# Performance work log

Measured on AMD Instinct MI355X. Metric: run time of the kernel, lower is better.

Reference implementation:

```python
import jax, jax.numpy as jnp
import numpy as np

# pool sizes (must match init_kwargs)
N_FQK, N_FV, N_REL, N_VAL, N_KNOW = 512, 256, 128, 32, 256
K_FQK, K_FV, K_REL, K_VAL = 64, 32, 16, 3
D_MODEL, D_SPACE = 1024, 64
B, S = 8, 2048


def _topk_sparsify(w, k):
    # keep top-k entries per row, zero the rest (values unchanged)
    vals, idx = jax.lax.top_k(w, k)                      # [B,k]
    out = jnp.zeros_like(w)
    rows = jnp.arange(w.shape[0])[:, None]
    return out.at[rows, idx].set(vals), idx


def setup_inputs() -> dict:
    key = jax.random.key(0)
    k1, k2, k3, k4 = jax.random.split(key, 4)
    x = jax.random.normal(k1, (B, S, D_MODEL), dtype=jnp.float32)
    # importance: per-token weights normalized over sequence
    importance = jax.nn.softmax(jax.random.normal(k2, (B, S), dtype=jnp.float32), axis=-1)
    W = jax.random.normal(k3, (D_MODEL, D_SPACE), dtype=jnp.float32) * 0.02
    b = jnp.zeros((D_SPACE,), dtype=jnp.float32)
    total = N_FQK + N_FV + N_REL + N_VAL + N_KNOW
    neuron_emb = jax.random.normal(k4, (total, D_SPACE), dtype=jnp.float32) * 0.02
    return {"x": x, "importance": importance, "W": W, "b": b, "neuron_emb": neuron_emb}


def reference(x, importance, W, b, neuron_emb):
    # projection (dropout inactive in eval); normalized neuron embeddings
    h = x @ W + b                                         # [B,S,d_space]
    emb_n = neuron_emb / jnp.linalg.norm(neuron_emb, axis=-1, keepdims=True)
    all_logits = jnp.einsum('bsd,nd->bsn', h, emb_n)      # [B,S,N_total]

    e0 = N_FQK
    e1 = e0 + N_FV
    e2 = e1 + N_REL
    e3 = e2 + N_VAL

    def route(lo, hi):
        pref = jax.nn.softmax(all_logits[..., lo:hi], axis=-1)  # [B,S,n]
        w = jnp.einsum('bs,bsn->bn', importance, pref)          # [B,n]
        return pref, w

    _, w_qk = route(0, e0)
    _, idx_qk = jax.lax.top_k(w_qk, K_FQK)
    idx_qk = jnp.sort(idx_qk, axis=-1)

    _, w_v = route(e0, e1)
    _, idx_v = jax.lax.top_k(w_v, K_FV)
    idx_v = jnp.sort(idx_v, axis=-1)

    # relational Q and K share the same logit slice (eval: no excitability bonus)
    _, w_rQ = route(e1, e2)
    _, w_rK = route(e1, e2)
    rw_Q, _ = _topk_sparsify(w_rQ, K_REL)
    rw_K, _ = _topk_sparsify(w_rK, K_REL)

    _, w_val = route(e2, e3)
    vw, _ = _topk_sparsify(w_val, K_VAL)

    return idx_qk, idx_v, rw_Q, rw_K, vw, w_qk, w_v
```

## Files before the change

kernel.cpp:

```cpp
#include <hip/hip_runtime.h>
#include <hip/hip_bf16.h>
#include <hip/hip_fp16.h>
#include <math.h>

#define ROWS  16384
#define DM    1024
#define DS    64
#define NUSE  928
#define NPAD  960
#define RPB   16
#define NBLK  (ROWS/RPB)

typedef __attribute__((ext_vector_type(8))) short bf16x8;
typedef __attribute__((ext_vector_type(4))) float f32x4;

static __device__ inline f32x4 mfma16(bf16x8 a, bf16x8 b, f32x4 c) {
    return __builtin_amdgcn_mfma_f32_16x16x32_bf16(a, b, c, 0, 0, 0);
}

static __device__ inline void bfsplit(float v, unsigned short& h, unsigned short& l) {
    unsigned u = __float_as_uint(v);
    unsigned hr = u + 0x7FFFu + ((u >> 16) & 1u);
    h = (unsigned short)(hr >> 16);
    float hf = __uint_as_float((unsigned)h << 16);
    float r = v - hf;
    unsigned ur = __float_as_uint(r);
    unsigned lr2 = ur + 0x7FFFu + ((ur >> 16) & 1u);
    l = (unsigned short)(lr2 >> 16);
}

#define OFF_EBH  0LL
#define OFF_EBL  122880LL
#define OFF_WBH  245760LL
#define OFF_WBL  376832LL
#define OFF_WP   507904LL

__global__ __launch_bounds__(256) void k_prep(const float* __restrict__ emb,
                                              const float* __restrict__ W,
                                              unsigned short* __restrict__ ebh,
                                              unsigned short* __restrict__ ebl,
                                              unsigned short* __restrict__ wbh,
                                              unsigned short* __restrict__ wbl) {
    if (blockIdx.x < 4) {
        int n = blockIdx.x * 256 + threadIdx.x;
        if (n >= NPAD) return;
        if (n >= NUSE) {
            #pragma unroll
            for (int d = 0; d < DS; d++) {
                int kt = d >> 5, q = (d >> 3) & 3, j = d & 7;
                int a = ((kt * 4 + q) * NPAD + n) * 8 + j;
                ebh[a] = 0; ebl[a] = 0;
            }
            return;
        }
        float ss = 0.f;
        #pragma unroll
        for (int d = 0; d < DS; d++) { float v = emb[n * DS + d]; ss = fmaf(v, v, ss); }
        float inv = 1.0f / sqrtf(ss);
        #pragma unroll
        for (int d = 0; d < DS; d++) {
            float v = emb[n * DS + d] * inv;
            unsigned short h, l; bfsplit(v, h, l);
            int kt = d >> 5, q = (d >> 3) & 3, j = d & 7;
            int a = ((kt * 4 + q) * NPAD + n) * 8 + j;
            ebh[a] = h; ebl[a] = l;
        }
    } else {
        int idx = (blockIdx.x - 4) * 256 + threadIdx.x;
        int ktg = idx >> 6, n = idx & 63;
        #pragma unroll
        for (int q = 0; q < 4; q++) {
            #pragma unroll
            for (int j = 0; j < 8; j++) {
                int k = ktg * 32 + q * 8 + j;
                float v = W[k * DS + n];
                unsigned short h, l; bfsplit(v, h, l);
                int a = ((ktg * 4 + q) * 64 + n) * 8 + j;
                wbh[a] = h; wbl[a] = l;
            }
        }
    }
}

__global__ __launch_bounds__(512, 8) void k_mega(const float* __restrict__ x,
                                                 const float* __restrict__ bias,
                                                 const unsigned short* __restrict__ wbh,
                                                 const unsigned short* __restrict__ wbl,
                                                 const unsigned short* __restrict__ ebh,
                                                 const unsigned short* __restrict__ ebl,
                                                 const float* __restrict__ imp,
                                                 float* __restrict__ wpart) {
    __shared__ __align__(16) unsigned char smem[40960];
    unsigned short* Ph   = (unsigned short*)smem;
    float*          Cb   = (float*)smem;
    unsigned short* Hh   = (unsigned short*)(smem + 34560);
    unsigned short* Hl   = (unsigned short*)(smem + 36608);
    float*          zslot = (float*)(smem + 38656);
    float*          coefL = (float*)(smem + 40704);

    const int tid = threadIdx.x;
    const int rc = blockIdx.x;
    const long long row0 = (long long)rc * RPB;
    const int w = tid >> 6, lane = tid & 63, q = lane >> 4, lm = lane & 15;

    zslot[tid] = 0.f;

    {
        const int kg = w;
        const float* xp = &x[(row0 + lm) * (long long)DM + kg * 128 + q * 8];
        f32x4 acc[4];
        #pragma unroll
        for (int f = 0; f < 4; f++) { acc[f].x = 0.f; acc[f].y = 0.f; acc[f].z = 0.f; acc[f].w = 0.f; }

        #pragma unroll
        for (int ks = 0; ks < 4; ks++) {
            float4 v0 = *(const float4*)&xp[ks * 32];
            float4 v1 = *(const float4*)&xp[ks * 32 + 4];
            union { bf16x8 v; unsigned short s[8]; } ah, al;
            bfsplit(v0.x, ah.s[0], al.s[0]); bfsplit(v0.y, ah.s[1], al.s[1]);
            bfsplit(v0.z, ah.s[2], al.s[2]); bfsplit(v0.w, ah.s[3], al.s[3]);
            bfsplit(v1.x, ah.s[4], al.s[4]); bfsplit(v1.y, ah.s[5], al.s[5]);
            bfsplit(v1.z, ah.s[6], al.s[6]); bfsplit(v1.w, ah.s[7], al.s[7]);
            const int ktg = kg * 4 + ks;
            #pragma unroll
            for (int f = 0; f < 4; f++) {
                const int ba = ((ktg * 4 + q) * 64 + f * 16 + lm) * 8;
                const bf16x8 b_h = *(const bf16x8*)&wbh[ba];
                const bf16x8 b_l = *(const bf16x8*)&wbl[ba];
                acc[f] = mfma16(ah.v, b_h, acc[f]);
                acc[f] = mfma16(ah.v, b_l, acc[f]);
                acc[f] = mfma16(al.v, b_h, acc[f]);
            }
        }
        #pragma unroll
        for (int f = 0; f < 4; f++)
            *(f32x4*)&Cb[(w * 64 + lane) * 16 + f * 4] = acc[f];
    }
    __syncthreads();

    #pragma unroll
    for (int ee = 0; ee < 2; ee++) {
        const int e = tid * 2 + ee;
        float s = 0.f;
        #pragma unroll
        for (int g = 0; g < 8; g++) s += Cb[g * 1024 + e];
        const int L = e >> 4, r = e & 15, f = r >> 2, t = r & 3;
        const int row = (L >> 4) * 4 + t;
        const int col = f * 16 + (L & 15);
        s += bias[col];
        unsigned short hh, ll; bfsplit(s, hh, ll);
        const int kt = col >> 5, qH = (col >> 3) & 3, j = col & 7;
        const int hidx = ((kt * 4 + qH) * RPB + row) * 8 + j;
        Hh[hidx] = hh; Hl[hidx] = ll;
    }
    __syncthreads();

    bf16x8 a_h[2], a_l[2];
    #pragma unroll
    for (int kt = 0; kt < 2; kt++) {
        const int ab = ((kt * 4 + q) * RPB + lm) * 8;
        a_h[kt] = *(const bf16x8*)&Hh[ab];
        a_l[kt] = *(const bf16x8*)&Hl[ab];
    }

    #pragma unroll
    for (int v = 0; v < 2; v++) {
        const int nt = w + v * 8;
        if (nt > 14) continue;
        f32x4 acc[4];
        #pragma unroll
        for (int f = 0; f < 4; f++) { acc[f].x = 0.f; acc[f].y = 0.f; acc[f].z = 0.f; acc[f].w = 0.f; }
        #pragma unroll
        for (int kt = 0; kt < 2; kt++) {
            #pragma unroll
            for (int f = 0; f < 4; f++) {
                const int bb = ((kt * 4 + q) * NPAD + nt * 64 + f * 16 + lm) * 8;
                const bf16x8 b_h = *(const bf16x8*)&ebh[bb];
                const bf16x8 b_l = *(const bf16x8*)&ebl[bb];
                acc[f] = mfma16(a_h[kt], b_h, acc[f]);
                acc[f] = mfma16(a_h[kt], b_l, acc[f]);
                acc[f] = mfma16(a_l[kt], b_h, acc[f]);
            }
        }
        const int sl = (nt < 8) ? 0 : (nt < 12) ? 1 : (nt < 14) ? 2 : 3;
        float s0 = 0.f, s1 = 0.f, s2 = 0.f, s3 = 0.f;
        #pragma unroll
        for (int f = 0; f < 4; f++) {
            float e0 = __expf(acc[f][0]);
            float e1 = __expf(acc[f][1]);
            float e2 = __expf(acc[f][2]);
            float e3 = __expf(acc[f][3]);
            const int n = nt * 64 + f * 16 + lm;
            unsigned short p0 = __half_as_ushort(__float2half(e0));
            unsigned short p1 = __half_as_ushort(__float2half(e1));
            unsigned short p2 = __half_as_ushort(__float2half(e2));
            unsigned short p3 = __half_as_ushort(__float2half(e3));
            *(unsigned*)&Ph[n * 18 + q * 4]     = (unsigned)p0 | ((unsigned)p1 << 16);
            *(unsigned*)&Ph[n * 18 + q * 4 + 2] = (unsigned)p2 | ((unsigned)p3 << 16);
            if (nt * 64 + f * 16 < NUSE) {
                s0 += e0; s1 += e1; s2 += e2; s3 += e3;
            }
        }
        #pragma unroll
        for (int off = 1; off < 16; off <<= 1) {
            s0 += __shfl_xor(s0, off); s1 += __shfl_xor(s1, off);
            s2 += __shfl_xor(s2, off); s3 += __shfl_xor(s3, off);
        }
        if (lm < 4) {
            float sv = (lm == 0) ? s0 : (lm == 1) ? s1 : (lm == 2) ? s2 : s3;
            zslot[(w * 4 + sl) * RPB + q * 4 + lm] += sv;
        }
    }
    __syncthreads();

    if (tid < RPB) {
        const int r = tid;
        const float im = imp[row0 + r];
        #pragma unroll
        for (int sl = 0; sl < 4; sl++) {
            float Z = 0.f;
            #pragma unroll
            for (int g = 0; g < 8; g++) Z += zslot[(g * 4 + sl) * RPB + r];
            coefL[r * 4 + sl] = im / Z;
        }
    }
    __syncthreads();

    for (int nn = tid; nn < NUSE; nn += 512) {
        const int sl = (nn < 512) ? 0 : (nn < 768) ? 1 : (nn < 896) ? 2 : 3;
        float acc = 0.f;
        #pragma unroll
        for (int rb = 0; rb < 8; rb++) {
            const unsigned pk = *(const unsigned*)&Ph[nn * 18 + rb * 2];
            float v0 = __half2float(__ushort_as_half((unsigned short)(pk & 0xFFFF)));
            float v1 = __half2float(__ushort_as_half((unsigned short)(pk >> 16)));
            acc = fmaf(coefL[(rb * 2 + 0) * 4 + sl], v0, acc);
            acc = fmaf(coefL[(rb * 2 + 1) * 4 + sl], v1, acc);
        }
        wpart[(long long)rc * NPAD + nn] = acc;
    }
}

__global__ __launch_bounds__(512) void k_out(const float* __restrict__ wpart,
                                             float* __restrict__ out) {
    const int b = blockIdx.x;
    const int tid = threadIdx.x;
    __shared__ float w_s[NUSE];
    __shared__ int   rk[NUSE];

    for (int n = tid; n < NUSE; n += 512) {
        float s = 0.f;
        #pragma unroll 4
        for (int c = 0; c < 128; c++)
            s += wpart[(long long)(b * 128 + c) * NPAD + n];
        w_s[n] = s;
        if (n < 512)      out[3072 + (long long)b * 512 + n] = s;
        else if (n < 768) out[7168 + (long long)b * 256 + (n - 512)] = s;
    }
    __syncthreads();

    for (int n = tid; n < NUSE; n += 512) {
        int lo, hi;
        if (n < 512)      { lo = 0;   hi = 512; }
        else if (n < 768) { lo = 512; hi = 768; }
        else if (n < 896) { lo = 768; hi = 896; }
        else              { lo = 896; hi = NUSE; }
        float wn = w_s[n];
        int r = 0;
        for (int m = lo; m < hi; m++) {
            float wm = w_s[m];
            r += (wm > wn) || ((wm == wn) && (m < n));
        }
        rk[n] = r;
    }
    __syncthreads();

    if (tid < 512) {
        int n = tid;
        if (rk[n] < 64) {
            int pos = 0;
            for (int m = 0; m < n; m++) pos += (rk[m] < 64) ? 1 : 0;
            out[(long long)b * 64 + pos] = (float)n;
        }
    }
    if (tid < 256) {
        int n = 512 + tid;
        if (rk[n] < 32) {
            int pos = 0;
            for (int m = 512; m < n; m++) pos += (rk[m] < 32) ? 1 : 0;
            out[512 + (long long)b * 32 + pos] = (float)tid;
        }
    }
    if (tid < 128) {
        int n = 768 + tid;
        float v = (rk[n] < 16) ? w_s[n] : 0.f;
        out[768 + (long long)b * 128 + tid] = v;
        out[1792 + (long long)b * 128 + tid] = v;
    }
    if (tid < 32) {
        int n = 896 + tid;
        float v = (rk[n] < 3) ? w_s[n] : 0.f;
        out[2816 + (long long)b * 32 + tid] = v;
    }
}

extern "C" void kernel_launch(void* const* d_in, const int* in_sizes, int n_in,
                              void* d_out, int out_size, void* d_ws, size_t ws_size,
                              hipStream_t stream) {
    const float* x    = (const float*)d_in[0];
    const float* imp  = (const float*)d_in[1];
    const float* W    = (const float*)d_in[2];
    const float* bias = (const float*)d_in[3];
    const float* emb  = (const float*)d_in[4];

    char* ws = (char*)d_ws;
    unsigned short* ebh = (unsigned short*)(ws + OFF_EBH);
    unsigned short* ebl = (unsigned short*)(ws + OFF_EBL);
    unsigned short* wbh = (unsigned short*)(ws + OFF_WBH);
    unsigned short* wbl = (unsigned short*)(ws + OFF_WBL);
    float* wpart        = (float*)(ws + OFF_WP);
    float* out          = (float*)d_out;

    k_prep<<<12, 256, 0, stream>>>(emb, W, ebh, ebl, wbh, wbl);
    k_mega<<<NBLK, 512, 0, stream>>>(x, bias, wbh, wbl, ebh, ebl, imp, wpart);
    k_out<<<8, 512, 0, stream>>>(wpart, out);
}
```

Baseline: 183.5 us.

## Parallelize partial-weight reduction into separate kernel and pad Cb smem layout

The cross-block reduction of per-block routing weights, previously done by only 8 blocks each serially summing 128 partials, moves to a new k_red kernel with a 29x8 grid and an in-block tree reduction. A separate k_rank kernel then does only the ranking and top-k output. The first-stage accumulator store to shared memory is rewritten to a padded row-major layout (stride 66) meant to cut bank conflicts in the 8-way k-group sum. The launch-bounds occupancy hint for k_mega drops from 8 to 4, loosening register limits. This adds one extra kernel launch and a small workspace buffer.

```diff
diff --git a/kernel.cpp b/kernel.cpp
--- a/kernel.cpp
+++ b/kernel.cpp
@@ -34,6 +34,7 @@
 #define OFF_WBH  245760LL
 #define OFF_WBL  376832LL
 #define OFF_WP   507904LL
+#define OFF_WR   4440064LL
 
 __global__ __launch_bounds__(256) void k_prep(const float* __restrict__ emb,
                                               const float* __restrict__ W,
@@ -82,7 +83,7 @@
     }
 }
 
-__global__ __launch_bounds__(512, 8) void k_mega(const float* __restrict__ x,
+__global__ __launch_bounds__(512, 4) void k_mega(const float* __restrict__ x,
                                                  const float* __restrict__ bias,
                                                  const unsigned short* __restrict__ wbh,
                                                  const unsigned short* __restrict__ wbl,
@@ -91,10 +92,10 @@
                                                  const float* __restrict__ imp,
                                                  float* __restrict__ wpart) {
     __shared__ __align__(16) unsigned char smem[40960];
-    unsigned short* Ph   = (unsigned short*)smem;
-    float*          Cb   = (float*)smem;
-    unsigned short* Hh   = (unsigned short*)(smem + 34560);
-    unsigned short* Hl   = (unsigned short*)(smem + 36608);
+    unsigned short* Ph    = (unsigned short*)smem;
+    float*          Cb    = (float*)smem;
+    unsigned short* Hh    = (unsigned short*)(smem + 34560);
+    unsigned short* Hl    = (unsigned short*)(smem + 36608);
     float*          zslot = (float*)(smem + 38656);
     float*          coefL = (float*)(smem + 40704);
 
@@ -134,23 +135,22 @@
         }
         #pragma unroll
         for (int f = 0; f < 4; f++)
-            *(f32x4*)&Cb[(w * 64 + lane) * 16 + f * 4] = acc[f];
+            #pragma unroll
+            for (int t = 0; t < 4; t++)
+                Cb[w * 1056 + (q * 4 + t) * 66 + f * 16 + lm] = acc[f][t];
     }
     __syncthreads();
 
     #pragma unroll
     for (int ee = 0; ee < 2; ee++) {
-        const int e = tid * 2 + ee;
-        float s = 0.f;
-        #pragma unroll
-        for (int g = 0; g < 8; g++) s += Cb[g * 1024 + e];
-        const int L = e >> 4, r = e & 15, f = r >> 2, t = r & 3;
-        const int row = (L >> 4) * 4 + t;
-        const int col = f * 16 + (L & 15);
-        s += bias[col];
+        const int e = tid + ee * 512;
+        const int row = e >> 6, col = e & 63;
+        float s = bias[col];
+        #pragma unroll
+        for (int g = 0; g < 8; g++) s += Cb[g * 1056 + row * 66 + col];
         unsigned short hh, ll; bfsplit(s, hh, ll);
-        const int kt = col >> 5, qH = (col >> 3) & 3, j = col & 7;
-        const int hidx = ((kt * 4 + qH) * RPB + row) * 8 + j;
+        const int kt = col >> 5, qH = (col >> 3) & 3, jH = col & 7;
+        const int hidx = ((kt * 4 + qH) * RPB + row) * 8 + jH;
         Hh[hidx] = hh; Hl[hidx] = ll;
     }
     __syncthreads();
@@ -167,9 +167,9 @@
     for (int v = 0; v < 2; v++) {
         const int nt = w + v * 8;
         if (nt > 14) continue;
-        f32x4 acc[4];
-        #pragma unroll
-        for (int f = 0; f < 4; f++) { acc[f].x = 0.f; acc[f].y = 0.f; acc[f].z = 0.f; acc[f].w = 0.f; }
+        f32x4 acc2[4];
+        #pragma unroll
+        for (int f = 0; f < 4; f++) { acc2[f].x = 0.f; acc2[f].y = 0.f; acc2[f].z = 0.f; acc2[f].w = 0.f; }
         #pragma unroll
         for (int kt = 0; kt < 2; kt++) {
             #pragma unroll
@@ -177,19 +177,19 @@
                 const int bb = ((kt * 4 + q) * NPAD + nt * 64 + f * 16 + lm) * 8;
                 const bf16x8 b_h = *(const bf16x8*)&ebh[bb];
                 const bf16x8 b_l = *(const bf16x8*)&ebl[bb];
-                acc[f] = mfma16(a_h[kt], b_h, acc[f]);
-                acc[f] = mfma16(a_h[kt], b_l, acc[f]);
-                acc[f] = mfma16(a_l[kt], b_h, acc[f]);
+                acc2[f] = mfma16(a_h[kt], b_h, acc2[f]);
+                acc2[f] = mfma16(a_h[kt], b_l, acc2[f]);
+                acc2[f] = mfma16(a_l[kt], b_h, acc2[f]);
             }
         }
         const int sl = (nt < 8) ? 0 : (nt < 12) ? 1 : (nt < 14) ? 2 : 3;
         float s0 = 0.f, s1 = 0.f, s2 = 0.f, s3 = 0.f;
         #pragma unroll
         for (int f = 0; f < 4; f++) {
-            float e0 = __expf(acc[f][0]);
-            float e1 = __expf(acc[f][1]);
-            float e2 = __expf(acc[f][2]);
-            float e3 = __expf(acc[f][3]);
+            float e0 = __expf(acc2[f][0]);
+            float e1 = __expf(acc2[f][1]);
+            float e2 = __expf(acc2[f][2]);
+            float e3 = __expf(acc2[f][3]);
             const int n = nt * 64 + f * 16 + lm;
             unsigned short p0 = __half_as_ushort(__float2half(e0));
             unsigned short p1 = __half_as_ushort(__float2half(e1));
@@ -228,31 +228,50 @@
 
     for (int nn = tid; nn < NUSE; nn += 512) {
         const int sl = (nn < 512) ? 0 : (nn < 768) ? 1 : (nn < 896) ? 2 : 3;
-        float acc = 0.f;
+        float accw = 0.f;
         #pragma unroll
         for (int rb = 0; rb < 8; rb++) {
             const unsigned pk = *(const unsigned*)&Ph[nn * 18 + rb * 2];
             float v0 = __half2float(__ushort_as_half((unsigned short)(pk & 0xFFFF)));
             float v1 = __half2float(__ushort_as_half((unsigned short)(pk >> 16)));
-            acc = fmaf(coefL[(rb * 2 + 0) * 4 + sl], v0, acc);
-            acc = fmaf(coefL[(rb * 2 + 1) * 4 + sl], v1, acc);
-        }
-        wpart[(long long)rc * NPAD + nn] = acc;
-    }
-}
-
-__global__ __launch_bounds__(512) void k_out(const float* __restrict__ wpart,
-                                             float* __restrict__ out) {
+            accw = fmaf(coefL[(rb * 2 + 0) * 4 + sl], v0, accw);
+            accw = fmaf(coefL[(rb * 2 + 1) * 4 + sl], v1, accw);
+        }
+        wpart[(long long)rc * NPAD + nn] = accw;
+    }
+}
+
+__global__ __launch_bounds__(256) void k_red(const float* __restrict__ wpart,
+                                             float* __restrict__ wred) {
+    const int g = blockIdx.x;
+    const int b = blockIdx.y;
+    const int tid = threadIdx.x;
+    const int n = g * 32 + (tid & 31);
+    const int cp = tid >> 5;
+    float s = 0.f;
+    #pragma unroll 2
+    for (int c = cp; c < 128; c += 8)
+        s += wpart[(long long)(b * 128 + c) * NPAD + n];
+    __shared__ float red[8][32];
+    red[cp][tid & 31] = s;
+    __syncthreads();
+    if (tid < 32) {
+        float t = 0.f;
+        #pragma unroll
+        for (int p = 0; p < 8; p++) t += red[p][tid];
+        wred[b * 960 + g * 32 + tid] = t;
+    }
+}
+
+__global__ __launch_bounds__(512) void k_rank(const float* __restrict__ wred,
+                                              float* __restrict__ out) {
     const int b = blockIdx.x;
     const int tid = threadIdx.x;
     __shared__ float w_s[NUSE];
     __shared__ int   rk[NUSE];
 
     for (int n = tid; n < NUSE; n += 512) {
-        float s = 0.f;
-        #pragma unroll 4
-        for (int c = 0; c < 128; c++)
-            s += wpart[(long long)(b * 128 + c) * NPAD + n];
+        float s = wred[b * 960 + n];
         w_s[n] = s;
         if (n < 512)      out[3072 + (long long)b * 512 + n] = s;
         else if (n < 768) out[7168 + (long long)b * 256 + (n - 512)] = s;
@@ -319,9 +338,11 @@
     unsigned short* wbh = (unsigned short*)(ws + OFF_WBH);
     unsigned short* wbl = (unsigned short*)(ws + OFF_WBL);
     float* wpart        = (float*)(ws + OFF_WP);
+    float* wred         = (float*)(ws + OFF_WR);
     float* out          = (float*)d_out;
 
     k_prep<<<12, 256, 0, stream>>>(emb, W, ebh, ebl, wbh, wbl);
     k_mega<<<NBLK, 512, 0, stream>>>(x, bias, wbh, wbl, ebh, ebl, imp, wpart);
-    k_out<<<8, 512, 0, stream>>>(wpart, out);
-}
+    k_red<<<dim3(29, 8), 256, 0, stream>>>(wpart, wred);
+    k_rank<<<8, 512, 0, stream>>>(wred, out);
+}
```

Result: faster. 164.5 us (-10.3%).
